# Kernel tuning notes

Hardware: AMD Instinct MI355X
Metric: run time of the kernel (lower is better)

The kernel has to match this reference:

```python
import jax, jax.numpy as jnp
import numpy as np

DIM = 192
HEADS = 4
CTX = 256
HID = int(DIM * 2.66)  # 510


def _dwconv(x, w):
    # x: (b,c,h,w), w: (c,1,3,3) depthwise
    return jax.lax.conv_general_dilated(
        x, w, window_strides=(1, 1), padding='SAME',
        dimension_numbers=('NCHW', 'OIHW', 'NCHW'),
        feature_group_count=x.shape[1])


def _conv1x1(x, w):
    # w: (out, in)
    return jnp.einsum('oc,bchw->bohw', w, x)


def _layernorm(x, weight, bias):
    # WithBias LayerNorm over channel dim (last dim after to_3d == channels)
    mu = x.mean(axis=1, keepdims=True)
    var = ((x - mu) ** 2).mean(axis=1, keepdims=True)
    xn = (x - mu) / jnp.sqrt(var + 1e-5)
    return xn * weight[None, :, None, None] + bias[None, :, None, None]


def setup_inputs() -> dict:
    key = jax.random.key(0)
    ks = jax.random.split(key, 16)
    s = 0.02
    inp = {
        'x': jax.random.normal(ks[0], (8, DIM, 128, 128), jnp.float32),
        'context_emb': jax.random.normal(ks[1], (8, CTX), jnp.float32),
        'ln1_w': jnp.ones((DIM,), jnp.float32),
        'ln1_b': jnp.zeros((DIM,), jnp.float32),
        'ln2_w': jnp.ones((DIM,), jnp.float32),
        'ln2_b': jnp.zeros((DIM,), jnp.float32),
        'w_qkv': jax.random.normal(ks[2], (3 * DIM, DIM), jnp.float32) * s,
        'w_qkv_dw': jax.random.normal(ks[3], (3 * DIM, 1, 3, 3), jnp.float32) * s,
        'w_proj': jax.random.normal(ks[4], (DIM, DIM), jnp.float32) * s,
        'base_temp': jnp.ones((HEADS, 1, 1), jnp.float32),
        'ta_w1': jax.random.normal(ks[5], (DIM // 4, CTX), jnp.float32) * s,
        'ta_b1': jnp.zeros((DIM // 4,), jnp.float32),
        'ta_w2': jax.random.normal(ks[6], (HEADS, DIM // 4), jnp.float32) * s,
        'ta_b2': jnp.zeros((HEADS,), jnp.float32),
        'vg_w': jax.random.normal(ks[7], (DIM, CTX), jnp.float32) * s,
        'vg_b': jnp.zeros((DIM,), jnp.float32),
        'w_local': jax.random.normal(ks[8], (DIM, 1, 3, 3), jnp.float32) * s,
        'w_ffn_in': jax.random.normal(ks[9], (2 * HID, DIM), jnp.float32) * s,
        'w_ffn_dw': jax.random.normal(ks[10], (2 * HID, 1, 3, 3), jnp.float32) * s,
        'w_ffn_out': jax.random.normal(ks[11], (DIM, HID), jnp.float32) * s,
    }
    return inp


def _forward(x, context_emb, ln1_w, ln1_b, ln2_w, ln2_b, w_qkv, w_qkv_dw,
             w_proj, base_temp, ta_w1, ta_b1, ta_w2, ta_b2, vg_w, vg_b,
             w_local, w_ffn_in, w_ffn_dw, w_ffn_out):
    b, c, h, w = x.shape
    hd = c // HEADS
    scale = hd ** (-0.5)

    # ---- Attention branch ----
    residual = x
    xn = _layernorm(x, ln1_w, ln1_b)

    # context adapters
    t = jax.nn.relu(context_emb @ ta_w1.T + ta_b1) @ ta_w2.T + ta_b2  # (b,heads)
    temp_factor = jax.nn.sigmoid(t)[:, :, None, None] * 2.0 + 0.5    # (b,heads,1,1)
    total_temp = base_temp[None] * temp_factor
    v_gate = jax.nn.sigmoid(context_emb @ vg_w.T + vg_b)             # (b,dim)
    v_gate = v_gate.reshape(b, HEADS, hd, 1)

    qkv = _dwconv(_conv1x1(xn, w_qkv), w_qkv_dw)
    q, k, v = jnp.split(qkv, 3, axis=1)

    def heads_flat(t4):
        return t4.reshape(b, HEADS, hd, h * w)

    qf = heads_flat(q)
    kf = heads_flat(k)
    vf = heads_flat(v)
    qf = qf / jnp.maximum(jnp.linalg.norm(qf, axis=-1, keepdims=True), 1e-12)
    kf = kf / jnp.maximum(jnp.linalg.norm(kf, axis=-1, keepdims=True), 1e-12)

    attn = jnp.einsum('bhcn,bhdn->bhcd', qf, kf) * scale  # (b,heads,hd,hd)
    attn = jax.nn.softmax(attn * total_temp, axis=-1)

    out_global = jnp.einsum('bhcd,bhdn->bhcn', attn, vf * v_gate)
    out_global = out_global.reshape(b, c, h, w)
    out_local = _dwconv(v, w_local)
    x = residual + _conv1x1(out_global + out_local, w_proj)

    # ---- GDFN branch ----
    residual = x
    xn = _layernorm(x, ln2_w, ln2_b)
    y = _dwconv(_conv1x1(xn, w_ffn_in), w_ffn_dw)
    y1, y2 = jnp.split(y, 2, axis=1)
    y = jax.nn.gelu(y1, approximate=False) * y2
    x = residual + _conv1x1(y, w_ffn_out)
    return x


def reference(x, context_emb, ln1_w, ln1_b, ln2_w, ln2_b, w_qkv, w_qkv_dw,
              w_proj, base_temp, ta_w1, ta_b1, ta_w2, ta_b2, vg_w, vg_b,
              w_local, w_ffn_in, w_ffn_dw, w_ffn_out):
    return _forward(x, context_emb, ln1_w, ln1_b, ln2_w, ln2_b, w_qkv,
                    w_qkv_dw, w_proj, base_temp, ta_w1, ta_b1, ta_w2, ta_b2,
                    vg_w, vg_b, w_local, w_ffn_in, w_ffn_dw, w_ffn_out)
```

## Files before the change

### kernel.cpp

```cpp
#include <hip/hip_runtime.h>
#include <math.h>

#define NB 8
#define NC 192
#define NH 128
#define NW 128
#define HW 16384
#define NQ 576
#define NHID 510
#define NHIDP 512
#define NG2 1020
#define NG2P 1024

#define BROWS 32
#define BSLOTS 34
#define BPIX (BSLOTS * NW)
#define BIPIX (BROWS * NW)

typedef unsigned short u16;
typedef short s16x8 __attribute__((ext_vector_type(8)));
typedef float f32x4 __attribute__((ext_vector_type(4)));

#define MFMA_BF16(a, b, c) __builtin_amdgcn_mfma_f32_16x16x32_bf16((a), (b), (c), 0, 0, 0)

__device__ __forceinline__ u16 f2bf(float f) {
  union { float f; unsigned u; } v; v.f = f;
  unsigned r = v.u + 0x7fffu + ((v.u >> 16) & 1u);
  return (u16)(r >> 16);
}
__device__ __forceinline__ float bf2f(u16 h) {
  union { unsigned u; float f; } v; v.u = ((unsigned)h) << 16; return v.f;
}
__device__ __forceinline__ float lo2f(unsigned u) {
  union { unsigned u; float f; } v; v.u = u << 16; return v.f;
}
__device__ __forceinline__ float hi2f(unsigned u) {
  union { unsigned u; float f; } v; v.u = u & 0xffff0000u; return v.f;
}

__device__ __forceinline__ void gll16(const void* g, void* l) {
  __builtin_amdgcn_global_load_lds(
      (const __attribute__((address_space(1))) void*)g,
      (__attribute__((address_space(3))) void*)l, 16, 0, 0);
}

__global__ void k_prep(const float* __restrict__ wq, const float* __restrict__ wfi,
                       const float* __restrict__ wfo,
                       u16* __restrict__ oq, u16* __restrict__ ofi, u16* __restrict__ ofo) {
  const int n1 = NQ * NC, n2 = NG2P * NC, n3 = NC * NHIDP;
  for (int i = blockIdx.x * blockDim.x + threadIdx.x; i < n1 + n2 + n3;
       i += gridDim.x * blockDim.x) {
    if (i < n1) {
      int row = i / NC, col = i - row * NC;
      int g = col >> 3, o = col & 7;
      int sc = (((g ^ (row & 7)) << 3) | o);
      oq[i] = f2bf(wq[row * NC + sc]);
    } else if (i < n1 + n2) {
      int j = i - n1; int row = j / NC, col = j - row * NC;
      int g = col >> 3, o = col & 7;
      int sc = (((g ^ (row & 7)) << 3) | o);
      u16 v = 0;
      if (row < NG2) v = f2bf(wfi[row * NC + sc]);
      ofi[j] = v;
    } else {
      int j = i - n1 - n2; int row = j >> 9, col = j & 511;
      u16 v = 0;
      if (col < NHID) v = f2bf(wfo[row * NHID + col]);
      ofo[j] = v;
    }
  }
}

__global__ void k_ctx(const float* __restrict__ ce, const float* __restrict__ taw1,
                      const float* __restrict__ tab1, const float* __restrict__ taw2,
                      const float* __restrict__ tab2, const float* __restrict__ vgw,
                      const float* __restrict__ vgb, const float* __restrict__ btemp,
                      float* __restrict__ tempt, float* __restrict__ vg) {
  int b = blockIdx.x, t = threadIdx.x;
  __shared__ float sce[256];
  __shared__ float shid[48];
  sce[t] = ce[b * 256 + t];
  __syncthreads();
  if (t < 48) {
    float s = tab1[t];
    for (int j = 0; j < 256; j++) s = fmaf(taw1[t * 256 + j], sce[j], s);
    shid[t] = fmaxf(s, 0.f);
  }
  __syncthreads();
  if (t < 4) {
    float s = tab2[t];
    for (int j = 0; j < 48; j++) s = fmaf(taw2[t * 48 + j], shid[j], s);
    float sg = 1.f / (1.f + expf(-s));
    tempt[b * 4 + t] = btemp[t] * (sg * 2.f + 0.5f);
  }
  if (t < 192) {
    float s = vgb[t];
    for (int j = 0; j < 256; j++) s = fmaf(vgw[t * 256 + j], sce[j], s);
    vg[b * 192 + t] = 1.f / (1.f + expf(-s));
  }
}

__global__ __launch_bounds__(256, 2)
void k_ln_gemm_band(const float* __restrict__ in, const float* __restrict__ lnw,
                    const float* __restrict__ lnb, const u16* __restrict__ wbf,
                    u16* __restrict__ out, int nchunks, int row_start, int slot0) {
  __shared__ u16 Xn[64 * 200];
  __shared__ u16 Wc[2][64 * 192];
  __shared__ float red[512];
  __shared__ float stats[128];
  int t = threadIdx.x;
  int lane = t & 63, wv = t >> 6;
  int bpb = gridDim.x >> 3;
  int b = blockIdx.x / bpb;
  int rb = blockIdx.x - b * bpb;
  int gpx0 = row_start * NW + rb * 64;
  int opx0 = slot0 * NW + rb * 64;
  const float* xp = in + (size_t)b * NC * HW + gpx0 + lane;
  float vals[48];
  float s = 0.f, s2 = 0.f;
#pragma unroll
  for (int j = 0; j < 48; j++) {
    float v = xp[(size_t)(wv * 48 + j) * HW];
    vals[j] = v; s += v; s2 = fmaf(v, v, s2);
  }
  red[wv * 64 + lane] = s;
  red[256 + wv * 64 + lane] = s2;
  __syncthreads();
  if (t < 64) {
    float m = 0.f, q = 0.f;
#pragma unroll
    for (int k = 0; k < 4; k++) { m += red[k * 64 + t]; q += red[256 + k * 64 + t]; }
    m *= (1.f / 192.f);
    float var = q * (1.f / 192.f) - m * m;
    stats[t] = m; stats[64 + t] = rsqrtf(var + 1e-5f);
  }
  __syncthreads();
  float mu = stats[lane], rs = stats[64 + lane];
#pragma unroll
  for (int j = 0; j < 48; j += 2) {
    int c = wv * 48 + j;
    float xa = (vals[j] - mu) * rs * lnw[c] + lnb[c];
    float xb = (vals[j + 1] - mu) * rs * lnw[c + 1] + lnb[c + 1];
    *(unsigned*)&Xn[lane * 200 + c] = (unsigned)f2bf(xa) | ((unsigned)f2bf(xb) << 16);
  }
  int r = lane & 15, grp = lane >> 4;
  int key = r & 7;
  int ostride = nchunks << 6;

  auto stageW = [&](int nc, int buf) {
    const u16* src = wbf + (size_t)nc * 64 * 192;
    for (int i = t; i < 1536; i += 256)
      gll16(&src[i * 8], &Wc[buf][i * 8]);
  };

  stageW(0, 0);
  __syncthreads();
  int cur = 0;
  for (int nc = 0; nc < nchunks; nc++) {
    if (nc + 1 < nchunks) stageW(nc + 1, cur ^ 1);
    f32x4 z = {0.f, 0.f, 0.f, 0.f};
    f32x4 acc0 = z, acc1 = z, acc2 = z, acc3 = z;
#pragma unroll
    for (int ks = 0; ks < 6; ks++) {
      int k0 = ks * 32 + grp * 8;
      int gsw = ((((ks << 2) + grp) ^ key) << 3);
      s16x8 a = *(s16x8*)&Xn[(wv * 16 + r) * 200 + k0];
      acc0 = MFMA_BF16(a, *(s16x8*)&Wc[cur][r * 192 + gsw], acc0);
      acc1 = MFMA_BF16(a, *(s16x8*)&Wc[cur][(16 + r) * 192 + gsw], acc1);
      acc2 = MFMA_BF16(a, *(s16x8*)&Wc[cur][(32 + r) * 192 + gsw], acc2);
      acc3 = MFMA_BF16(a, *(s16x8*)&Wc[cur][(48 + r) * 192 + gsw], acc3);
    }
    u16* op = out + ((size_t)b * BPIX + opx0 + wv * 16 + grp * 4) * ostride + nc * 64 + r;
#pragma unroll
    for (int i = 0; i < 4; i++) {
      op[(size_t)i * ostride] = f2bf(acc0[i]);
      op[(size_t)i * ostride + 16] = f2bf(acc1[i]);
      op[(size_t)i * ostride + 32] = f2bf(acc2[i]);
      op[(size_t)i * ostride + 48] = f2bf(acc3[i]);
    }
    __syncthreads();
    cur ^= 1;
  }
}

__global__ __launch_bounds__(256, 4)
void k_dw_attn_band(const u16* __restrict__ qb_band, const float* __restrict__ wdw,
                    u16* __restrict__ qkb, u16* __restrict__ vpm,
                    float* __restrict__ ssq, int r0, const u16* __restrict__ zp) {
  __shared__ u16 Hl[6 * 18 * 64];
  __shared__ float sred[8 * 64];
  int t = threadIdx.x;
  int cc = blockIdx.x % 9;
  int rem = blockIdx.x / 9;
  int b = rem >> 6; int r2 = rem & 63;
  int h0l = (r2 >> 3) * 4, w0 = (r2 & 7) * 16;
  int c0 = cc * 64;
  const s16x8 z8 = {0, 0, 0, 0, 0, 0, 0, 0};
  for (int i = t; i < 864; i += 256) {
    int px = i >> 3, sg = i & 7;
    int hh = px / 18, ww = px % 18;
    int slot = h0l + hh;
    int gh = r0 - 1 + slot;
    int gw = w0 - 1 + ww;
    const void* g = (gh >= 0 && gh < NH && gw >= 0 && gw < NW)
        ? (const void*)&qb_band[((size_t)b * BPIX + slot * NW + gw) * NQ + c0 + sg * 8]
        : (const void*)zp;
    gll16(g, &Hl[i * 8]);
  }
  __syncthreads();
  int cp = t & 31, psub = t >> 5;
  int pr = psub >> 1, pc0 = (psub & 1) * 8;
  int gc = c0 + 2 * cp;
  float wg0[9], wg1[9];
#pragma unroll
  for (int q = 0; q < 9; q++) { wg0[q] = wdw[gc * 9 + q]; wg1[q] = wdw[(gc + 1) * 9 + q]; }
  bool isv = (c0 >= 384);
  float sq0 = 0.f, sq1 = 0.f;
  s16x8 ov0 = z8, ov1 = z8;
#pragma unroll
  for (int j = 0; j < 8; j++) {
    int pc = pc0 + j;
    float a0 = 0.f, a1 = 0.f;
#pragma unroll
    for (int dr = 0; dr < 3; dr++)
#pragma unroll
      for (int dc = 0; dc < 3; dc++) {
        unsigned u = *(const unsigned*)&Hl[((pr + dr) * 18 + pc + dc) * 64 + 2 * cp];
        a0 = fmaf(lo2f(u), wg0[dr * 3 + dc], a0);
        a1 = fmaf(hi2f(u), wg1[dr * 3 + dc], a1);
      }
    u16 u0 = f2bf(a0), u1 = f2bf(a1);
    if (isv) {
      int gp = (r0 + h0l + pr) * NW + w0 + pc;
      *(unsigned*)&vpm[((size_t)b * HW + gp) * 192 + (gc - 384)] =
          (unsigned)u0 | ((unsigned)u1 << 16);
    } else {
      ov0[j] = (short)u0; ov1[j] = (short)u1;
      float f0 = bf2f(u0), f1 = bf2f(u1);
      sq0 = fmaf(f0, f0, sq0); sq1 = fmaf(f1, f1, sq1);
    }
  }
  if (!isv) {
    int lpx = (h0l + pr) * NW + w0 + pc0;
    *(s16x8*)&qkb[((size_t)b * 384 + gc) * BIPIX + lpx] = ov0;
    *(s16x8*)&qkb[((size_t)b * 384 + gc + 1) * BIPIX + lpx] = ov1;
    sred[psub * 64 + 2 * cp] = sq0;
    sred[psub * 64 + 2 * cp + 1] = sq1;
    __syncthreads();
    if (t < 64) {
      float sa = 0.f;
#pragma unroll
      for (int p8 = 0; p8 < 8; p8++) sa += sred[p8 * 64 + t];
      atomicAdd(&ssq[b * 384 + c0 + t], sa);
    }
  }
}

__global__ __launch_bounds__(256, 2)
void k_attn_band(const u16* __restrict__ qkb, float* __restrict__ attn) {
  __shared__ float par[4 * 2304];
  int t = threadIdx.x;
  int lane = t & 63, wv = t >> 6;
  int r = lane & 15, grp = lane >> 4;
  int bh = blockIdx.x >> 2, kc = blockIdx.x & 3;
  int b = bh >> 2, h = bh & 3;
  const u16* qb = qkb + ((size_t)b * 384 + h * 48) * BIPIX;
  const u16* kb = qkb + ((size_t)b * 384 + 192 + h * 48) * BIPIX;
  f32x4 z = {0.f, 0.f, 0.f, 0.f};
  f32x4 acc[3][3];
#pragma unroll
  for (int i = 0; i < 3; i++)
#pragma unroll
    for (int j = 0; j < 3; j++) acc[i][j] = z;
  int kbase = kc * 1024 + wv * 256 + grp * 8;
#pragma unroll 2
  for (int ks = 0; ks < 8; ks++) {
    int k0 = kbase + ks * 32;
    s16x8 af[3], bf[3];
#pragma unroll
    for (int mt = 0; mt < 3; mt++) af[mt] = *(const s16x8*)&qb[(size_t)(mt * 16 + r) * BIPIX + k0];
#pragma unroll
    for (int nt = 0; nt < 3; nt++) bf[nt] = *(const s16x8*)&kb[(size_t)(nt * 16 + r) * BIPIX + k0];
#pragma unroll
    for (int mt = 0; mt < 3; mt++)
#pragma unroll
      for (int nt = 0; nt < 3; nt++) acc[mt][nt] = MFMA_BF16(af[mt], bf[nt], acc[mt][nt]);
  }
#pragma unroll
  for (int mt = 0; mt < 3; mt++)
#pragma unroll
    for (int nt = 0; nt < 3; nt++)
#pragma unroll
      for (int i = 0; i < 4; i++)
        par[wv * 2304 + (mt * 16 + grp * 4 + i) * 48 + nt * 16 + r] = acc[mt][nt][i];
  __syncthreads();
  float* ag = attn + (size_t)bh * 2304;
  for (int i = t; i < 2304; i += 256)
    atomicAdd(&ag[i], par[i] + par[2304 + i] + par[4608 + i] + par[6912 + i]);
}

__global__ void k_softmax(float* __restrict__ attn, const float* __restrict__ ssq,
                          const float* __restrict__ tempt, const float* __restrict__ vg) {
  int bh = blockIdx.x, b = bh >> 2, h = bh & 3;
  int t = threadIdx.x;
  __shared__ float srk[48], svg[48];
  if (t < 48) {
    float nk = sqrtf(ssq[b * 384 + 192 + h * 48 + t]);
    srk[t] = 1.f / fmaxf(nk, 1e-12f);
    svg[t] = vg[b * 192 + h * 48 + t];
  }
  __syncthreads();
  if (t < 48) {
    float nq = sqrtf(ssq[b * 384 + h * 48 + t]);
    float rq = 1.f / fmaxf(nq, 1e-12f);
    float sc = 0.14433756729740643f * tempt[b * 4 + h] * rq;
    float* row = attn + (size_t)bh * 2304 + t * 48;
    float l[48]; float mx = -1e30f;
#pragma unroll
    for (int d = 0; d < 48; d++) { l[d] = row[d] * srk[d] * sc; mx = fmaxf(mx, l[d]); }
    float ss = 0.f;
#pragma unroll
    for (int d = 0; d < 48; d++) { l[d] = expf(l[d] - mx); ss += l[d]; }
    float inv = 1.f / ss;
#pragma unroll
    for (int d = 0; d < 48; d++) row[d] = l[d] * inv * svg[d];
  }
}

__global__ __launch_bounds__(256)
void k_wd(const float* __restrict__ attn, const float* __restrict__ wp,
          u16* __restrict__ wdg) {
  __shared__ float am[4 * 48 * 48];
  int b = blockIdx.x >> 3, oc = blockIdx.x & 7;
  int t = threadIdx.x;
  const float* ag = attn + (size_t)b * 4 * 2304;
  for (int i = t; i < 9216; i += 256) am[i] = ag[i];
  __syncthreads();
  u16* wdb = wdg + (size_t)b * 192 * 384;
  for (int idx = t; idx < 24 * 384; idx += 256) {
    int oo = idx / 384, j = idx % 384;
    int o = oc * 24 + oo;
    float val;
    if (j < 192) {
      int hj = j / 48, dj = j % 48;
      const float* wpo = wp + o * 192 + hj * 48;
      const float* ap = am + hj * 2304 + dj;
      float sa = 0.f;
#pragma unroll
      for (int c = 0; c < 48; c++) sa = fmaf(wpo[c], ap[c * 48], sa);
      val = sa;
    } else {
      val = wp[o * 192 + (j - 192)];
    }
    wdb[o * 384 + j] = f2bf(val);
  }
}

__global__ __launch_bounds__(256, 2)
void k_proj(const u16* __restrict__ vpm, const float* __restrict__ wl,
            const u16* __restrict__ wdg, const float* __restrict__ x,
            float* __restrict__ x2, const u16* __restrict__ zp) {
  __shared__ u16 Hl[2][6 * 18 * 64];
  __shared__ u16 Xl[64 * 392];
  int t = threadIdx.x;
  int b = blockIdx.x >> 8; int r2 = blockIdx.x & 255;
  int h0 = (r2 >> 3) * 4, w0 = (r2 & 7) * 16;
  int cp = t & 31, psub = t >> 5;
  int pr = psub >> 1, pc0 = (psub & 1) * 8;
  int lane = t & 63, wv = t >> 6;
  int r = lane & 15, grp = lane >> 4;

  auto stageH = [&](int c3s, int buf) {
    int c0s = c3s * 64;
    for (int i = t; i < 864; i += 256) {
      int px = i >> 3, sg = i & 7;
      int hh = px / 18, ww = px % 18;
      int gh = h0 - 1 + hh, gw = w0 - 1 + ww;
      const void* g = (gh >= 0 && gh < NH && gw >= 0 && gw < NW)
          ? (const void*)&vpm[((size_t)b * HW + gh * NW + gw) * 192 + c0s + sg * 8]
          : (const void*)zp;
      gll16(g, &Hl[buf][i * 8]);
    }
  };

  stageH(0, 0);
  __syncthreads();
  int cur = 0;
  for (int c3 = 0; c3 < 3; c3++) {
    if (c3 < 2) stageH(c3 + 1, cur ^ 1);
    int c0 = c3 * 64;
    int gc = c0 + 2 * cp;
    float wg0[9], wg1[9];
#pragma unroll
    for (int q = 0; q < 9; q++) { wg0[q] = wl[gc * 9 + q]; wg1[q] = wl[(gc + 1) * 9 + q]; }
#pragma unroll
    for (int j = 0; j < 8; j++) {
      int pc = pc0 + j; int p = pr * 16 + pc;
      float a0 = 0.f, a1 = 0.f; unsigned uc = 0;
#pragma unroll
      for (int dr = 0; dr < 3; dr++)
#pragma unroll
        for (int dc = 0; dc < 3; dc++) {
          unsigned u = *(const unsigned*)&Hl[cur][((pr + dr) * 18 + pc + dc) * 64 + 2 * cp];
          if (dr == 1 && dc == 1) uc = u;
          a0 = fmaf(lo2f(u), wg0[dr * 3 + dc], a0);
          a1 = fmaf(hi2f(u), wg1[dr * 3 + dc], a1);
        }
      *(unsigned*)&Xl[p * 392 + gc] = uc;
      *(unsigned*)&Xl[p * 392 + 192 + gc] =
          (unsigned)f2bf(a0) | ((unsigned)f2bf(a1) << 16);
    }
    __syncthreads();
    cur ^= 1;
  }
  float xres[3][4][4];
#pragma unroll
  for (int mt = 0; mt < 3; mt++)
#pragma unroll
    for (int nt = 0; nt < 4; nt++) {
      size_t base = ((size_t)b * NC + wv * 48 + mt * 16 + grp * 4) * HW +
                    (h0 + nt) * NW + w0 + r;
#pragma unroll
      for (int i = 0; i < 4; i++) xres[mt][nt][i] = x[base + (size_t)i * HW];
    }
#pragma unroll
  for (int mt = 0; mt < 3; mt++)
#pragma unroll
    for (int nt = 0; nt < 4; nt++)
#pragma unroll
      for (int i = 0; i < 4; i++)
        asm volatile("" : "+v"(xres[mt][nt][i]));

  const u16* wdb = wdg + (size_t)b * 192 * 384;
  f32x4 z = {0.f, 0.f, 0.f, 0.f};
  f32x4 acc[3][4];
#pragma unroll
  for (int i = 0; i < 3; i++)
#pragma unroll
    for (int j = 0; j < 4; j++) acc[i][j] = z;
#pragma unroll 2
  for (int ks = 0; ks < 12; ks++) {
    int k0 = ks * 32 + grp * 8;
    s16x8 b0 = *(s16x8*)&Xl[r * 392 + k0];
    s16x8 b1 = *(s16x8*)&Xl[(16 + r) * 392 + k0];
    s16x8 b2 = *(s16x8*)&Xl[(32 + r) * 392 + k0];
    s16x8 b3 = *(s16x8*)&Xl[(48 + r) * 392 + k0];
#pragma unroll
    for (int mt = 0; mt < 3; mt++) {
      s16x8 a = *(const s16x8*)&wdb[(size_t)(wv * 48 + mt * 16 + r) * 384 + k0];
      acc[mt][0] = MFMA_BF16(a, b0, acc[mt][0]);
      acc[mt][1] = MFMA_BF16(a, b1, acc[mt][1]);
      acc[mt][2] = MFMA_BF16(a, b2, acc[mt][2]);
      acc[mt][3] = MFMA_BF16(a, b3, acc[mt][3]);
    }
  }
#pragma unroll
  for (int mt = 0; mt < 3; mt++)
#pragma unroll
    for (int nt = 0; nt < 4; nt++) {
      size_t base = ((size_t)b * NC + wv * 48 + mt * 16 + grp * 4) * HW +
                    (h0 + nt) * NW + w0 + r;
#pragma unroll
      for (int i = 0; i < 4; i++) {
        size_t idx = base + (size_t)i * HW;
        x2[idx] = acc[mt][nt][i] + xres[mt][nt][i];
      }
    }
}

__global__ __launch_bounds__(256, 2)
void k_gelu_ffn_band(const u16* __restrict__ ypre, const float* __restrict__ wdwf,
                     const u16* __restrict__ wfo, const float* __restrict__ x2,
                     float* __restrict__ out, int r0, const u16* __restrict__ zp) {
  __shared__ u16 H1[2][6 * 18 * 64];
  __shared__ u16 H2[2][6 * 18 * 72];
  __shared__ u16 Yc[64 * 80];
  int t = threadIdx.x;
  int b = blockIdx.x >> 6; int r2 = blockIdx.x & 63;
  int h0l = (r2 >> 3) * 4, w0 = (r2 & 7) * 16;
  int cp = t & 31, psub = t >> 5;
  int pr = psub >> 1, pc0 = (psub & 1) * 8;
  int lane = t & 63, wv = t >> 6;
  int r = lane & 15, grp = lane >> 4;
  int jl = 2 * cp;

  auto stage = [&](int jc, int buf) {
    int j0s = jc * 64;
    int base2 = j0s + 504;
    for (int i = t; i < 864; i += 256) {
      int px = i >> 3, sg = i & 7;
      int hh = px / 18, ww = px % 18;
      int slot = h0l + hh;
      int gh = r0 - 1 + slot, gw = w0 - 1 + ww;
      const void* g = (gh >= 0 && gh < NH && gw >= 0 && gw < NW)
          ? (const void*)&ypre[((size_t)b * BPIX + slot * NW + gw) * NG2P + j0s + sg * 8]
          : (const void*)zp;
      gll16(g, &H1[buf][i * 8]);
    }
    for (int i = t; i < 972; i += 256) {
      int px = i / 9, sg = i - px * 9;
      int hh = px / 18, ww = px % 18;
      int slot = h0l + hh;
      int gh = r0 - 1 + slot, gw = w0 - 1 + ww;
      const void* g = (gh >= 0 && gh < NH && gw >= 0 && gw < NW)
          ? (const void*)&ypre[((size_t)b * BPIX + slot * NW + gw) * NG2P + base2 + sg * 8]
          : (const void*)zp;
      gll16(g, &H2[buf][i * 8]);
    }
  };

  f32x4 z = {0.f, 0.f, 0.f, 0.f};
  f32x4 acc[3][4];
#pragma unroll
  for (int i = 0; i < 3; i++)
#pragma unroll
    for (int j = 0; j < 4; j++) acc[i][j] = z;

  stage(0, 0);
  __syncthreads();
  int cur = 0;
  for (int jc = 0; jc < 8; jc++) {
    if (jc < 7) stage(jc + 1, cur ^ 1);
    int j0 = jc * 64;
    int j = j0 + jl;
    bool v0 = (j < NHID), v1 = (j + 1 < NHID);
    float w1a[9], w1b[9], w2a[9], w2b[9];
#pragma unroll
    for (int q = 0; q < 9; q++) {
      w1a[q] = 0.f; w1b[q] = 0.f; w2a[q] = 0.f; w2b[q] = 0.f;
      if (v0) { w1a[q] = wdwf[j * 9 + q]; w2a[q] = wdwf[(j + NHID) * 9 + q]; }
      if (v1) { w1b[q] = wdwf[(j + 1) * 9 + q]; w2b[q] = wdwf[(j + 1 + NHID) * 9 + q]; }
    }
#pragma unroll
    for (int jj = 0; jj < 8; jj++) {
      int pc = pc0 + jj;
      float d1a = 0.f, d1b = 0.f, d2a = 0.f, d2b = 0.f;
#pragma unroll
      for (int dr = 0; dr < 3; dr++)
#pragma unroll
        for (int dc = 0; dc < 3; dc++) {
          int q = dr * 3 + dc;
          unsigned u1 = *(const unsigned*)&H1[cur][((pr + dr) * 18 + pc + dc) * 64 + jl];
          unsigned u2 = *(const unsigned*)&H2[cur][((pr + dr) * 18 + pc + dc) * 72 + jl + 6];
          d1a = fmaf(lo2f(u1), w1a[q], d1a); d1b = fmaf(hi2f(u1), w1b[q], d1b);
          d2a = fmaf(lo2f(u2), w2a[q], d2a); d2b = fmaf(hi2f(u2), w2b[q], d2b);
        }
      float ga = 0.5f * d1a * (1.f + erff(d1a * 0.70710678118654752f));
      float gb = 0.5f * d1b * (1.f + erff(d1b * 0.70710678118654752f));
      float ya = v0 ? ga * d2a : 0.f;
      float yb = v1 ? gb * d2b : 0.f;
      int lp = pr * 16 + pc;
      *(unsigned*)&Yc[lp * 80 + jl] = (unsigned)f2bf(ya) | ((unsigned)f2bf(yb) << 16);
    }
    __syncthreads();
#pragma unroll
    for (int ks = 0; ks < 2; ks++) {
      int k0 = ks * 32 + grp * 8;
      s16x8 b0 = *(s16x8*)&Yc[r * 80 + k0];
      s16x8 b1 = *(s16x8*)&Yc[(16 + r) * 80 + k0];
      s16x8 b2 = *(s16x8*)&Yc[(32 + r) * 80 + k0];
      s16x8 b3 = *(s16x8*)&Yc[(48 + r) * 80 + k0];
#pragma unroll
      for (int mt = 0; mt < 3; mt++) {
        s16x8 a = *(const s16x8*)&wfo[(size_t)(wv * 48 + mt * 16 + r) * NHIDP + j0 + k0];
        acc[mt][0] = MFMA_BF16(a, b0, acc[mt][0]);
        acc[mt][1] = MFMA_BF16(a, b1, acc[mt][1]);
        acc[mt][2] = MFMA_BF16(a, b2, acc[mt][2]);
        acc[mt][3] = MFMA_BF16(a, b3, acc[mt][3]);
      }
    }
    __syncthreads();
    cur ^= 1;
  }
#pragma unroll
  for (int mt = 0; mt < 3; mt++)
#pragma unroll
    for (int nt = 0; nt < 4; nt++) {
      size_t base = ((size_t)b * NC + wv * 48 + mt * 16 + grp * 4) * HW +
                    (r0 + h0l + nt) * NW + w0 + r;
#pragma unroll
      for (int i = 0; i < 4; i++) {
        size_t idx = base + (size_t)i * HW;
        out[idx] = acc[mt][nt][i] + x2[idx];
      }
    }
}

extern "C" void kernel_launch(void* const* d_in, const int* in_sizes, int n_in,
                              void* d_out, int out_size, void* d_ws, size_t ws_size,
                              hipStream_t stream) {
  const float* x      = (const float*)d_in[0];
  const float* ce     = (const float*)d_in[1];
  const float* ln1w   = (const float*)d_in[2];
  const float* ln1b   = (const float*)d_in[3];
  const float* ln2w   = (const float*)d_in[4];
  const float* ln2b   = (const float*)d_in[5];
  const float* wqkv   = (const float*)d_in[6];
  const float* wqkvdw = (const float*)d_in[7];
  const float* wproj  = (const float*)d_in[8];
  const float* btemp  = (const float*)d_in[9];
  const float* taw1   = (const float*)d_in[10];
  const float* tab1   = (const float*)d_in[11];
  const float* taw2   = (const float*)d_in[12];
  const float* tab2   = (const float*)d_in[13];
  const float* vgw    = (const float*)d_in[14];
  const float* vgb    = (const float*)d_in[15];
  const float* wlocal = (const float*)d_in[16];
  const float* wffni  = (const float*)d_in[17];
  const float* wffndw = (const float*)d_in[18];
  const float* wffno  = (const float*)d_in[19];
  float* outp = (float*)d_out;
  char* ws = (char*)d_ws;

  const size_t REQUIRED = 224602496ULL;
  if (ws_size < REQUIRED) {
    hipMemsetAsync(d_out, 0, (size_t)out_size * 4, stream);
    return;
  }
  u16*   wq_bf   = (u16*)(ws + 0);
  u16*   wfi_bf  = (u16*)(ws + 221184);
  u16*   wfo_bf  = (u16*)(ws + 614400);
  float* tempt   = (float*)(ws + 811008);
  float* vg      = (float*)(ws + 811136);
  float* ssq     = (float*)(ws + 817280);
  float* attn    = (float*)(ws + 829568);
  u16*   wdg     = (u16*)(ws + 1124480);
  u16*   qkvband = (u16*)(ws + 2304128);
  u16*   qkband  = (u16*)(ws + 42412160);
  u16*   ypreband= (u16*)(ws + 2304128);
  u16*   vpm     = (u16*)(ws + 73607296);
  float* x2      = (float*)(ws + 123938944);
  u16*   zp      = (u16*)(ws + 224602240);

  hipMemsetAsync(ws + 817280, 0, 12288 + 294912, stream);
  hipMemsetAsync(ws + 224602240, 0, 256, stream);
  k_prep<<<512, 256, 0, stream>>>(wqkv, wffni, wffno, wq_bf, wfi_bf, wfo_bf);
  k_ctx<<<8, 256, 0, stream>>>(ce, taw1, tab1, taw2, tab2, vgw, vgb, btemp, tempt, vg);

  for (int band = 0; band < 4; band++) {
    int r0 = band * BROWS;
    int rs = (r0 > 0) ? r0 - 1 : 0;
    int re = (r0 + BROWS + 1 < NH) ? r0 + BROWS + 1 : NH;
    int nr = re - rs;
    int s0 = rs - (r0 - 1);
    k_ln_gemm_band<<<8 * nr * 2, 256, 0, stream>>>(x, ln1w, ln1b, wq_bf, qkvband, 9, rs, s0);
    k_dw_attn_band<<<9 * 8 * 64, 256, 0, stream>>>(qkvband, wqkvdw, qkband, vpm, ssq, r0, zp);
    k_attn_band<<<32 * 4, 256, 0, stream>>>(qkband, attn);
  }
  k_softmax<<<32, 64, 0, stream>>>(attn, ssq, tempt, vg);
  k_wd<<<64, 256, 0, stream>>>(attn, wproj, wdg);
  k_proj<<<2048, 256, 0, stream>>>(vpm, wlocal, wdg, x, x2, zp);

  for (int band = 0; band < 4; band++) {
    int r0 = band * BROWS;
    int rs = (r0 > 0) ? r0 - 1 : 0;
    int re = (r0 + BROWS + 1 < NH) ? r0 + BROWS + 1 : NH;
    int nr = re - rs;
    int s0 = rs - (r0 - 1);
    k_ln_gemm_band<<<8 * nr * 2, 256, 0, stream>>>(x2, ln2w, ln2b, wfi_bf, ypreband, 16, rs, s0);
    k_gelu_ffn_band<<<8 * 64, 256, 0, stream>>>(ypreband, wffndw, wfo_bf, x2, outp, r0, zp);
  }
}
```

Baseline: 1.077 ms.

## Store projection output as bf16 delta, recompute residual; swizzle blocks across XCDs

The fp32 intermediate x2 is no longer materialised. k_proj now writes only the projection output as packed bf16 pairs, and the LN2 GEMM and FFN epilogue rebuild x + proj on the fly. This halves the traffic for that intermediate and removes the fp32 residual read in k_proj, at the cost of bf16 rounding on the attention branch contribution. Block indices are also remapped so consecutive work lands on the same XCD, and k_attn_band splits K into 8 chunks instead of 4 for more parallelism.

```diff
diff --git a/kernel.cpp b/kernel.cpp
--- a/kernel.cpp
+++ b/kernel.cpp
@@ -36,6 +36,12 @@
 }
 __device__ __forceinline__ float hi2f(unsigned u) {
   union { unsigned u; float f; } v; v.u = u & 0xffff0000u; return v.f;
+}
+__device__ __forceinline__ unsigned pack2(float a, float b) {
+  return (unsigned)f2bf(a) | ((unsigned)f2bf(b) << 16);
+}
+__device__ __forceinline__ int xcdswz(int bid, int nwg) {
+  return (bid & 7) * (nwg >> 3) + (bid >> 3);
 }
 
 __device__ __forceinline__ void gll16(const void* g, void* l) {
@@ -101,7 +107,8 @@
 }
 
 __global__ __launch_bounds__(256, 2)
-void k_ln_gemm_band(const float* __restrict__ in, const float* __restrict__ lnw,
+void k_ln_gemm_band(const float* __restrict__ in, const unsigned* __restrict__ res,
+                    const float* __restrict__ lnw,
                     const float* __restrict__ lnb, const u16* __restrict__ wbf,
                     u16* __restrict__ out, int nchunks, int row_start, int slot0) {
   __shared__ u16 Xn[64 * 200];
@@ -111,17 +118,26 @@
   int t = threadIdx.x;
   int lane = t & 63, wv = t >> 6;
   int bpb = gridDim.x >> 3;
-  int b = blockIdx.x / bpb;
-  int rb = blockIdx.x - b * bpb;
+  int nb = xcdswz(blockIdx.x, gridDim.x);
+  int b = nb / bpb;
+  int rb = nb - b * bpb;
   int gpx0 = row_start * NW + rb * 64;
   int opx0 = slot0 * NW + rb * 64;
   const float* xp = in + (size_t)b * NC * HW + gpx0 + lane;
+  const unsigned* rp = res + (size_t)b * 96 * HW + gpx0 + lane;
+  bool hasres = (res != nullptr);
   float vals[48];
   float s = 0.f, s2 = 0.f;
 #pragma unroll
-  for (int j = 0; j < 48; j++) {
-    float v = xp[(size_t)(wv * 48 + j) * HW];
-    vals[j] = v; s += v; s2 = fmaf(v, v, s2);
+  for (int j = 0; j < 48; j += 2) {
+    float v0 = xp[(size_t)(wv * 48 + j) * HW];
+    float v1 = xp[(size_t)(wv * 48 + j + 1) * HW];
+    if (hasres) {
+      unsigned pr = rp[(size_t)(wv * 24 + (j >> 1)) * HW];
+      v0 += lo2f(pr); v1 += hi2f(pr);
+    }
+    vals[j] = v0; vals[j + 1] = v1;
+    s += v0 + v1; s2 = fmaf(v0, v0, s2); s2 = fmaf(v1, v1, s2);
   }
   red[wv * 64 + lane] = s;
   red[256 + wv * 64 + lane] = s2;
@@ -141,7 +157,7 @@
     int c = wv * 48 + j;
     float xa = (vals[j] - mu) * rs * lnw[c] + lnb[c];
     float xb = (vals[j + 1] - mu) * rs * lnw[c + 1] + lnb[c + 1];
-    *(unsigned*)&Xn[lane * 200 + c] = (unsigned)f2bf(xa) | ((unsigned)f2bf(xb) << 16);
+    *(unsigned*)&Xn[lane * 200 + c] = pack2(xa, xb);
   }
   int r = lane & 15, grp = lane >> 4;
   int key = r & 7;
@@ -190,8 +206,9 @@
   __shared__ u16 Hl[6 * 18 * 64];
   __shared__ float sred[8 * 64];
   int t = threadIdx.x;
-  int cc = blockIdx.x % 9;
-  int rem = blockIdx.x / 9;
+  int nb = xcdswz(blockIdx.x, gridDim.x);
+  int cc = nb % 9;
+  int rem = nb / 9;
   int b = rem >> 6; int r2 = rem & 63;
   int h0l = (r2 >> 3) * 4, w0 = (r2 & 7) * 16;
   int c0 = cc * 64;
@@ -262,7 +279,8 @@
   int t = threadIdx.x;
   int lane = t & 63, wv = t >> 6;
   int r = lane & 15, grp = lane >> 4;
-  int bh = blockIdx.x >> 2, kc = blockIdx.x & 3;
+  int nb = xcdswz(blockIdx.x, gridDim.x);
+  int bh = nb >> 3, kc = nb & 7;
   int b = bh >> 2, h = bh & 3;
   const u16* qb = qkb + ((size_t)b * 384 + h * 48) * BIPIX;
   const u16* kb = qkb + ((size_t)b * 384 + 192 + h * 48) * BIPIX;
@@ -272,9 +290,9 @@
   for (int i = 0; i < 3; i++)
 #pragma unroll
     for (int j = 0; j < 3; j++) acc[i][j] = z;
-  int kbase = kc * 1024 + wv * 256 + grp * 8;
-#pragma unroll 2
-  for (int ks = 0; ks < 8; ks++) {
+  int kbase = kc * 512 + wv * 128 + grp * 8;
+#pragma unroll
+  for (int ks = 0; ks < 4; ks++) {
     int k0 = kbase + ks * 32;
     s16x8 af[3], bf[3];
 #pragma unroll
@@ -358,12 +376,13 @@
 
 __global__ __launch_bounds__(256, 2)
 void k_proj(const u16* __restrict__ vpm, const float* __restrict__ wl,
-            const u16* __restrict__ wdg, const float* __restrict__ x,
-            float* __restrict__ x2, const u16* __restrict__ zp) {
+            const u16* __restrict__ wdg, unsigned* __restrict__ proj,
+            const u16* __restrict__ zp) {
   __shared__ u16 Hl[2][6 * 18 * 64];
   __shared__ u16 Xl[64 * 392];
   int t = threadIdx.x;
-  int b = blockIdx.x >> 8; int r2 = blockIdx.x & 255;
+  int nb = xcdswz(blockIdx.x, gridDim.x);
+  int b = nb >> 8; int r2 = nb & 255;
   int h0 = (r2 >> 3) * 4, w0 = (r2 & 7) * 16;
   int cp = t & 31, psub = t >> 5;
   int pr = psub >> 1, pc0 = (psub & 1) * 8;
@@ -407,30 +426,11 @@
           a1 = fmaf(hi2f(u), wg1[dr * 3 + dc], a1);
         }
       *(unsigned*)&Xl[p * 392 + gc] = uc;
-      *(unsigned*)&Xl[p * 392 + 192 + gc] =
-          (unsigned)f2bf(a0) | ((unsigned)f2bf(a1) << 16);
+      *(unsigned*)&Xl[p * 392 + 192 + gc] = pack2(a0, a1);
     }
     __syncthreads();
     cur ^= 1;
   }
-  float xres[3][4][4];
-#pragma unroll
-  for (int mt = 0; mt < 3; mt++)
-#pragma unroll
-    for (int nt = 0; nt < 4; nt++) {
-      size_t base = ((size_t)b * NC + wv * 48 + mt * 16 + grp * 4) * HW +
-                    (h0 + nt) * NW + w0 + r;
-#pragma unroll
-      for (int i = 0; i < 4; i++) xres[mt][nt][i] = x[base + (size_t)i * HW];
-    }
-#pragma unroll
-  for (int mt = 0; mt < 3; mt++)
-#pragma unroll
-    for (int nt = 0; nt < 4; nt++)
-#pragma unroll
-      for (int i = 0; i < 4; i++)
-        asm volatile("" : "+v"(xres[mt][nt][i]));
-
   const u16* wdb = wdg + (size_t)b * 192 * 384;
   f32x4 z = {0.f, 0.f, 0.f, 0.f};
   f32x4 acc[3][4];
@@ -458,25 +458,24 @@
   for (int mt = 0; mt < 3; mt++)
 #pragma unroll
     for (int nt = 0; nt < 4; nt++) {
-      size_t base = ((size_t)b * NC + wv * 48 + mt * 16 + grp * 4) * HW +
-                    (h0 + nt) * NW + w0 + r;
-#pragma unroll
-      for (int i = 0; i < 4; i++) {
-        size_t idx = base + (size_t)i * HW;
-        x2[idx] = acc[mt][nt][i] + xres[mt][nt][i];
-      }
+      int cpair = wv * 24 + mt * 8 + grp * 2;
+      size_t pb = ((size_t)b * 96 + cpair) * HW + (h0 + nt) * NW + w0 + r;
+      proj[pb] = pack2(acc[mt][nt][0], acc[mt][nt][1]);
+      proj[pb + HW] = pack2(acc[mt][nt][2], acc[mt][nt][3]);
     }
 }
 
 __global__ __launch_bounds__(256, 2)
 void k_gelu_ffn_band(const u16* __restrict__ ypre, const float* __restrict__ wdwf,
-                     const u16* __restrict__ wfo, const float* __restrict__ x2,
+                     const u16* __restrict__ wfo, const float* __restrict__ x,
+                     const unsigned* __restrict__ proj,
                      float* __restrict__ out, int r0, const u16* __restrict__ zp) {
   __shared__ u16 H1[2][6 * 18 * 64];
   __shared__ u16 H2[2][6 * 18 * 72];
   __shared__ u16 Yc[64 * 80];
   int t = threadIdx.x;
-  int b = blockIdx.x >> 6; int r2 = blockIdx.x & 63;
+  int nb = xcdswz(blockIdx.x, gridDim.x);
+  int b = nb >> 6; int r2 = nb & 63;
   int h0l = (r2 >> 3) * 4, w0 = (r2 & 7) * 16;
   int cp = t & 31, psub = t >> 5;
   int pr = psub >> 1, pc0 = (psub & 1) * 8;
@@ -550,7 +549,7 @@
       float ya = v0 ? ga * d2a : 0.f;
       float yb = v1 ? gb * d2b : 0.f;
       int lp = pr * 16 + pc;
-      *(unsigned*)&Yc[lp * 80 + jl] = (unsigned)f2bf(ya) | ((unsigned)f2bf(yb) << 16);
+      *(unsigned*)&Yc[lp * 80 + jl] = pack2(ya, yb);
     }
     __syncthreads();
 #pragma unroll
@@ -578,11 +577,13 @@
     for (int nt = 0; nt < 4; nt++) {
       size_t base = ((size_t)b * NC + wv * 48 + mt * 16 + grp * 4) * HW +
                     (r0 + h0l + nt) * NW + w0 + r;
-#pragma unroll
-      for (int i = 0; i < 4; i++) {
-        size_t idx = base + (size_t)i * HW;
-        out[idx] = acc[mt][nt][i] + x2[idx];
-      }
+      int cpair = wv * 24 + mt * 8 + grp * 2;
+      size_t pb = ((size_t)b * 96 + cpair) * HW + (r0 + h0l + nt) * NW + w0 + r;
+      unsigned p0 = proj[pb], p1 = proj[pb + HW];
+      out[base] = acc[mt][nt][0] + x[base] + lo2f(p0);
+      out[base + HW] = acc[mt][nt][1] + x[base + HW] + hi2f(p0);
+      out[base + 2 * (size_t)HW] = acc[mt][nt][2] + x[base + 2 * (size_t)HW] + lo2f(p1);
+      out[base + 3 * (size_t)HW] = acc[mt][nt][3] + x[base + 3 * (size_t)HW] + hi2f(p1);
     }
 }
 
@@ -612,7 +613,7 @@
   float* outp = (float*)d_out;
   char* ws = (char*)d_ws;
 
-  const size_t REQUIRED = 224602496ULL;
+  const size_t REQUIRED = 174270848ULL;
   if (ws_size < REQUIRED) {
     hipMemsetAsync(d_out, 0, (size_t)out_size * 4, stream);
     return;
@@ -629,11 +630,11 @@
   u16*   qkband  = (u16*)(ws + 42412160);
   u16*   ypreband= (u16*)(ws + 2304128);
   u16*   vpm     = (u16*)(ws + 73607296);
-  float* x2      = (float*)(ws + 123938944);
-  u16*   zp      = (u16*)(ws + 224602240);
+  unsigned* proj = (unsigned*)(ws + 123938944);
+  u16*   zp      = (u16*)(ws + 174270592);
 
   hipMemsetAsync(ws + 817280, 0, 12288 + 294912, stream);
-  hipMemsetAsync(ws + 224602240, 0, 256, stream);
+  hipMemsetAsync(ws + 174270592, 0, 256, stream);
   k_prep<<<512, 256, 0, stream>>>(wqkv, wffni, wffno, wq_bf, wfi_bf, wfo_bf);
   k_ctx<<<8, 256, 0, stream>>>(ce, taw1, tab1, taw2, tab2, vgw, vgb, btemp, tempt, vg);
 
@@ -643,13 +644,14 @@
     int re = (r0 + BROWS + 1 < NH) ? r0 + BROWS + 1 : NH;
     int nr = re - rs;
     int s0 = rs - (r0 - 1);
-    k_ln_gemm_band<<<8 * nr * 2, 256, 0, stream>>>(x, ln1w, ln1b, wq_bf, qkvband, 9, rs, s0);
+    k_ln_gemm_band<<<8 * nr * 2, 256, 0, stream>>>(x, nullptr, ln1w, ln1b, wq_bf,
+                                                   qkvband, 9, rs, s0);
     k_dw_attn_band<<<9 * 8 * 64, 256, 0, stream>>>(qkvband, wqkvdw, qkband, vpm, ssq, r0, zp);
-    k_attn_band<<<32 * 4, 256, 0, stream>>>(qkband, attn);
+    k_attn_band<<<32 * 8, 256, 0, stream>>>(qkband, attn);
   }
   k_softmax<<<32, 64, 0, stream>>>(attn, ssq, tempt, vg);
   k_wd<<<64, 256, 0, stream>>>(attn, wproj, wdg);
-  k_proj<<<2048, 256, 0, stream>>>(vpm, wlocal, wdg, x, x2, zp);
+  k_proj<<<2048, 256, 0, stream>>>(vpm, wlocal, wdg, proj, zp);
 
   for (int band = 0; band < 4; band++) {
     int r0 = band * BROWS;
@@ -657,7 +659,9 @@
     int re = (r0 + BROWS + 1 < NH) ? r0 + BROWS + 1 : NH;
     int nr = re - rs;
     int s0 = rs - (r0 - 1);
-    k_ln_gemm_band<<<8 * nr * 2, 256, 0, stream>>>(x2, ln2w, ln2b, wfi_bf, ypreband, 16, rs, s0);
-    k_gelu_ffn_band<<<8 * 64, 256, 0, stream>>>(ypreband, wffndw, wfo_bf, x2, outp, r0, zp);
-  }
-}
+    k_ln_gemm_band<<<8 * nr * 2, 256, 0, stream>>>(x, proj, ln2w, ln2b, wfi_bf,
+                                                   ypreband, 16, rs, s0);
+    k_gelu_ffn_band<<<8 * 64, 256, 0, stream>>>(ypreband, wffndw, wfo_bf, x, proj,
+                                                outp, r0, zp);
+  }
+}
```

Result: no change. 1.096 ms (+1.8%).
